# Kernel optimization log

Hardware: AMD Instinct MI355X
Metric: run time of the kernel (lower is better)

The kernel has to match this reference:

```python
import jax, jax.numpy as jnp
import numpy as np

B, T, D, K = 4, 4096, 384, 64

def setup_inputs() -> dict:
    key = jax.random.key(0)
    k1, k2, k3, k4 = jax.random.split(key, 4)
    x = jax.random.normal(k1, (B, T, D), dtype=jnp.float32)
    # nn.Linear weights stored as (out_features, in_features); y = x @ W.T
    Wk = jax.random.normal(k2, (K, D), dtype=jnp.float32) * (1.0 / np.sqrt(D))
    Wq = jax.random.normal(k3, (K, D), dtype=jnp.float32) * (1.0 / np.sqrt(D))
    Wv = jax.random.normal(k4, (D, D), dtype=jnp.float32) * (1.0 / np.sqrt(D))
    return {"x": x, "Wk": Wk, "Wq": Wq, "Wv": Wv}

def reference(x, Wk, Wq, Wv):
    # x: (B,T,D)
    k = jnp.einsum('btd,kd->btk', x, Wk)   # (B,T,K)
    q = jnp.einsum('btd,kd->btk', x, Wq)   # (B,T,K)
    v = jnp.einsum('btd,ed->bte', x, Wv)   # (B,T,D)
    scores = jnp.einsum('btk,bsk->bts', q, k)  # (B,T,T)
    Tq = x.shape[1]
    causal = jnp.tril(jnp.ones((Tq, Tq), dtype=bool))[None, :, :]
    scores = jnp.where(causal, scores, -jnp.inf)
    w = jax.nn.softmax(scores / jnp.sqrt(jnp.asarray(Wk.shape[0], scores.dtype)), axis=-1)
    return jnp.einsum('bts,bsd->btd', w, v)  # (B,T,D)
```

## Files before the change

### kernel.cpp

```cpp
#include <hip/hip_runtime.h>


#define BB 4
#define TT 4096
#define DD 384

#define OWKA 0
#define OWQA 24576
#define OWVB 49152
#define OYK  196608
#define OYQ  1245184
#define OVT  2293760

#define C_EXP 0.18033688011112042f

typedef __bf16 bf16x8 __attribute__((ext_vector_type(8)));
typedef float f32x16 __attribute__((ext_vector_type(16)));
typedef unsigned short u16x4 __attribute__((ext_vector_type(4)));

__device__ __forceinline__ unsigned short f2bf(float f) {
  unsigned int u = __builtin_bit_cast(unsigned int, f);
  u += 0x7FFFu + ((u >> 16) & 1u);
  return (unsigned short)(u >> 16);
}

__device__ __forceinline__ bf16x8 ldb8(const unsigned short* p) {
  return *reinterpret_cast<const bf16x8*>(p);
}

__global__ __launch_bounds__(256) void convert_w(
    const float* __restrict__ Wk, const float* __restrict__ Wq,
    const float* __restrict__ Wv, unsigned short* __restrict__ ws) {
  int g = blockIdx.x * 256 + threadIdx.x;
  int row = g / 96;
  int fin = (g - row * 96) * 4;
  const float* src;
  unsigned short* dstbase;
  int m;
  if (row < 64)       { src = Wk + row * 384;         dstbase = ws + OWKA; m = row; }
  else if (row < 128) { src = Wq + (row - 64) * 384;  dstbase = ws + OWQA; m = row - 64; }
  else                { src = Wv + (row - 128) * 384; dstbase = ws + OWVB; m = row - 128; }
  float4 f = *reinterpret_cast<const float4*>(src + fin);
  u16x4 o;
  o[0] = f2bf(f.x); o[1] = f2bf(f.y); o[2] = f2bf(f.z); o[3] = f2bf(f.w);
  unsigned short* dst = dstbase + (m >> 5) * 12288 + (fin >> 4) * 512
                        + ((((fin >> 3) & 1) << 5) + (m & 31)) * 8 + (fin & 7);
  *reinterpret_cast<u16x4*>(dst) = o;
}

__global__ __launch_bounds__(512) void proj_fused(
    const float* __restrict__ x, const unsigned short* __restrict__ ws_r,
    unsigned short* __restrict__ Yk, unsigned short* __restrict__ Yq,
    unsigned short* __restrict__ Vt) {
  __shared__ __align__(16) unsigned short xlds[12288];
  int tb2 = blockIdx.x;
  int b = tb2 >> 7;
  int tt = tb2 & 127;
  int tid = threadIdx.x;
  {
    const float* xb = x + tb2 * 12288;
#pragma unroll
    for (int j = 0; j < 6; j++) {
      int v = tid + 512 * j;
      int r = v / 96;
      int fin = (v - r * 96) * 4;
      float4 f = *reinterpret_cast<const float4*>(xb + v * 4);
      u16x4 o;
      o[0] = f2bf(f.x); o[1] = f2bf(f.y); o[2] = f2bf(f.z); o[3] = f2bf(f.w);
      unsigned short* dst = xlds + (fin >> 4) * 512
                            + ((((fin >> 3) & 1) << 5) + r) * 8 + (fin & 7);
      *reinterpret_cast<u16x4*>(dst) = o;
    }
  }
  __syncthreads();
  int wid = tid >> 6, lane = tid & 63;
  int l31 = lane & 31, h8 = lane >> 5;
  const f32x16 fz16 = {};
  if (wid < 2) {
    const unsigned short* Wa = ws_r + (wid ? OWQA : OWKA) + lane * 8;
    unsigned short* Ysel = (wid ? Yq : Yk);
    f32x16 acc0 = fz16, acc1 = fz16;
    bf16x8 cw0[8], cw1[8], nw0[8], nw1[8];
#pragma unroll
    for (int i = 0; i < 8; i++) {
      cw0[i] = ldb8(Wa + i * 512);
      cw1[i] = ldb8(Wa + 12288 + i * 512);
    }
    asm volatile("" ::: "memory");
#pragma unroll
    for (int c = 0; c < 3; c++) {
      if (c < 2) {
#pragma unroll
        for (int i = 0; i < 8; i++) {
          nw0[i] = ldb8(Wa + (c + 1) * 4096 + i * 512);
          nw1[i] = ldb8(Wa + 12288 + (c + 1) * 4096 + i * 512);
        }
        asm volatile("" ::: "memory");
      }
#pragma unroll
      for (int i = 0; i < 8; i++) {
        bf16x8 b0 = ldb8(xlds + (c * 8 + i) * 512 + lane * 8);
        acc0 = __builtin_amdgcn_mfma_f32_32x32x16_bf16(cw0[i], b0, acc0, 0, 0, 0);
        acc1 = __builtin_amdgcn_mfma_f32_32x32x16_bf16(cw1[i], b0, acc1, 0, 0, 0);
      }
      if (c < 2) {
#pragma unroll
        for (int i = 0; i < 8; i++) { cw0[i] = nw0[i]; cw1[i] = nw1[i]; }
      }
    }
    int tile = b * 128 + tt;
    f32x16 am[2] = {acc0, acc1};
#pragma unroll
    for (int mt = 0; mt < 2; mt++)
#pragma unroll
      for (int rg = 0; rg < 4; rg++) {
        u16x4 o;
#pragma unroll
        for (int i = 0; i < 4; i++) o[i] = f2bf(am[mt][rg * 4 + i]);
        *reinterpret_cast<u16x4*>(Ysel + tile * 2048 + (mt * 2 + (rg >> 1)) * 512
                                  + (((rg & 1) << 5) + l31) * 8 + 4 * h8) = o;
      }
  } else {
    int vw = wid - 2;
    const unsigned short* Wb = ws_r + OWVB + vw * 2 * 12288 + lane * 8;
    f32x16 acc0 = fz16, acc1 = fz16;
    bf16x8 cw0[8], cw1[8], nw0[8], nw1[8];
#pragma unroll
    for (int i = 0; i < 8; i++) {
      cw0[i] = ldb8(Wb + i * 512);
      cw1[i] = ldb8(Wb + 12288 + i * 512);
    }
    asm volatile("" ::: "memory");
#pragma unroll
    for (int c = 0; c < 3; c++) {
      if (c < 2) {
#pragma unroll
        for (int i = 0; i < 8; i++) {
          nw0[i] = ldb8(Wb + (c + 1) * 4096 + i * 512);
          nw1[i] = ldb8(Wb + 12288 + (c + 1) * 4096 + i * 512);
        }
        asm volatile("" ::: "memory");
      }
#pragma unroll
      for (int i = 0; i < 8; i++) {
        bf16x8 a0 = ldb8(xlds + (c * 8 + i) * 512 + lane * 8);
        acc0 = __builtin_amdgcn_mfma_f32_32x32x16_bf16(a0, cw0[i], acc0, 0, 0, 0);
        acc1 = __builtin_amdgcn_mfma_f32_32x32x16_bf16(a0, cw1[i], acc1, 0, 0, 0);
      }
      if (c < 2) {
#pragma unroll
        for (int i = 0; i < 8; i++) { cw0[i] = nw0[i]; cw1[i] = nw1[i]; }
      }
    }
    int k128 = tt >> 2;
    int ks0 = (tb2 & 3) * 2;
    f32x16 ad[2] = {acc0, acc1};
#pragma unroll
    for (int dt = 0; dt < 2; dt++) {
      int dti = vw * 2 + dt;
      unsigned short* vbase = Vt + ((b * 12 + dti) * 32 + k128) * 4096;
#pragma unroll
      for (int rg = 0; rg < 4; rg++) {
        u16x4 o;
#pragma unroll
        for (int i = 0; i < 4; i++) o[i] = f2bf(ad[dt][rg * 4 + i]);
        int kseg = ks0 + (rg >> 1);
        *reinterpret_cast<u16x4*>(vbase + kseg * 512
                                  + (((rg & 1) << 5) + l31) * 8 + 4 * h8) = o;
      }
    }
  }
}

__global__ __launch_bounds__(256, 2) void flash_attn(
    const unsigned short* __restrict__ Yk, const unsigned short* __restrict__ Yq,
    const unsigned short* __restrict__ Vt, float* __restrict__ out) {
  __shared__ __align__(16) unsigned short pbuf[2][8192];
  __shared__ float lred[4][32];
  int blk = blockIdx.x;
  int xcd = blk & 7;
  int b = xcd >> 1, half = xcd & 1;
  int n = blk >> 3;
  int st = (n < 32) ? (127 - 2 * n - half) : (2 * (n - 32) + half);
  int wid = threadIdx.x >> 6, lane = threadIdx.x & 63;
  int l31 = lane & 31, h8 = lane >> 5;
  const f32x16 fz16 = {};
  const unsigned short* qbase = Yq + (b * 128 + st) * 2048 + lane * 8;
  bf16x8 qf[4];
#pragma unroll
  for (int ks = 0; ks < 4; ks++) qf[ks] = ldb8(qbase + ks * 512);
  f32x16 acc[3];
  acc[0] = fz16; acc[1] = fz16; acc[2] = fz16;
  float psum = 0.f;
  int n128 = (st >> 2) + 1;
  int qrow = st * 32 + l31;
  const unsigned short* kbase = Yk + (b * 128 + wid) * 2048 + lane * 8;
  const unsigned short* vbase = Vt + ((b * 12 + wid * 3) * 32) * 4096 + lane * 8;
#pragma unroll 1
  for (int kb = 0; kb < n128; kb++) {
    const unsigned short* kt = kbase + kb * 8192;
    bf16x8 kf[4];
#pragma unroll
    for (int ks = 0; ks < 4; ks++) kf[ks] = ldb8(kt + ks * 512);
    f32x16 sacc = fz16;
#pragma unroll
    for (int ks = 0; ks < 4; ks++)
      sacc = __builtin_amdgcn_mfma_f32_32x32x16_bf16(kf[ks], qf[ks], sacc, 0, 0, 0);
    int kg0 = kb * 128 + wid * 32 + 4 * h8;
    unsigned short* pw = pbuf[kb & 1];
#pragma unroll
    for (int rg = 0; rg < 4; rg++) {
      u16x4 o;
#pragma unroll
      for (int i = 0; i < 4; i++) {
        int key = kg0 + rg * 8 + i;
        float pv = (key > qrow) ? 0.f : exp2f(sacc[rg * 4 + i] * C_EXP);
        psum += pv;
        o[i] = f2bf(pv);
      }
      int g = wid * 2 + (rg >> 1);
      *reinterpret_cast<u16x4*>(pw + g * 512 + ((rg & 1) * 32 + l31) * 8 + 4 * h8) = o;
    }
    const unsigned short* vt = vbase + kb * 4096;
    bf16x8 vf0[8], vf1[8], vf2[8];
#pragma unroll
    for (int g = 0; g < 8; g++) vf0[g] = ldb8(vt + g * 512);
#pragma unroll
    for (int g = 0; g < 8; g++) vf1[g] = ldb8(vt + 32 * 4096 + g * 512);
#pragma unroll
    for (int g = 0; g < 8; g++) vf2[g] = ldb8(vt + 64 * 4096 + g * 512);
    __syncthreads();
    bf16x8 pf[8];
#pragma unroll
    for (int g = 0; g < 8; g++) pf[g] = ldb8(pw + g * 512 + lane * 8);
#pragma unroll
    for (int g = 0; g < 8; g++) {
      acc[0] = __builtin_amdgcn_mfma_f32_32x32x16_bf16(vf0[g], pf[g], acc[0], 0, 0, 0);
      acc[1] = __builtin_amdgcn_mfma_f32_32x32x16_bf16(vf1[g], pf[g], acc[1], 0, 0, 0);
      acc[2] = __builtin_amdgcn_mfma_f32_32x32x16_bf16(vf2[g], pf[g], acc[2], 0, 0, 0);
    }
  }
  psum += __shfl_xor(psum, 32);
  if (h8 == 0) lred[wid][l31] = psum;
  __syncthreads();
  float lt = lred[0][l31] + lred[1][l31] + lred[2][l31] + lred[3][l31];
  float inv = 1.0f / lt;
  float* ob = out + (b * TT + st * 32 + l31) * DD + wid * 96;
#pragma unroll
  for (int dt = 0; dt < 3; dt++)
#pragma unroll
    for (int rg = 0; rg < 4; rg++) {
      float4 o4;
      o4.x = acc[dt][rg * 4 + 0] * inv; o4.y = acc[dt][rg * 4 + 1] * inv;
      o4.z = acc[dt][rg * 4 + 2] * inv; o4.w = acc[dt][rg * 4 + 3] * inv;
      *reinterpret_cast<float4*>(ob + dt * 32 + rg * 8 + h8 * 4) = o4;
    }
}

extern "C" void kernel_launch(void* const* d_in, const int* in_sizes, int n_in,
                              void* d_out, int out_size, void* d_ws, size_t ws_size,
                              hipStream_t stream) {
  const float* x  = (const float*)d_in[0];
  const float* Wk = (const float*)d_in[1];
  const float* Wq = (const float*)d_in[2];
  const float* Wv = (const float*)d_in[3];
  unsigned short* ws = (unsigned short*)d_ws;
  unsigned short* Yk = ws + OYK;
  unsigned short* Yq = ws + OYQ;
  unsigned short* Vt = ws + OVT;

  convert_w<<<192, 256, 0, stream>>>(Wk, Wq, Wv, ws);
  proj_fused<<<512, 512, 0, stream>>>(x, ws, Yk, Yq, Vt);
  flash_attn<<<512, 256, 0, stream>>>(Yk, Yq, Vt, (float*)d_out);
}
```

Measured before the change: 149.3 us.

## Software-pipeline K and V global loads one key block ahead in attention loop

Loads K and V fragments for the first key block before the loop, then issues the next block's K loads after the score MFMAs and the next block's V loads after the PV MFMAs. This keeps global-memory latency off the critical path of each iteration. It also swaps __syncthreads for an explicit lgkmcnt wait plus s_barrier, so the barrier no longer waits on outstanding global loads. In exchange it keeps many more registers live (double-buffered K and V fragments), which may lower occupancy, and it does one redundant reload on the last iteration.

```diff
diff --git a/kernel.cpp b/kernel.cpp
--- a/kernel.cpp
+++ b/kernel.cpp
@@ -196,16 +196,29 @@
   int qrow = st * 32 + l31;
   const unsigned short* kbase = Yk + (b * 128 + wid) * 2048 + lane * 8;
   const unsigned short* vbase = Vt + ((b * 12 + wid * 3) * 32) * 4096 + lane * 8;
+  bf16x8 kf[4];
+#pragma unroll
+  for (int ks = 0; ks < 4; ks++) kf[ks] = ldb8(kbase + ks * 512);
+  bf16x8 vf0[8], vf1[8], vf2[8];
+#pragma unroll
+  for (int g = 0; g < 8; g++) vf0[g] = ldb8(vbase + g * 512);
+#pragma unroll
+  for (int g = 0; g < 8; g++) vf1[g] = ldb8(vbase + 32 * 4096 + g * 512);
+#pragma unroll
+  for (int g = 0; g < 8; g++) vf2[g] = ldb8(vbase + 64 * 4096 + g * 512);
+  asm volatile("" ::: "memory");
 #pragma unroll 1
   for (int kb = 0; kb < n128; kb++) {
-    const unsigned short* kt = kbase + kb * 8192;
-    bf16x8 kf[4];
-#pragma unroll
-    for (int ks = 0; ks < 4; ks++) kf[ks] = ldb8(kt + ks * 512);
     f32x16 sacc = fz16;
 #pragma unroll
     for (int ks = 0; ks < 4; ks++)
       sacc = __builtin_amdgcn_mfma_f32_32x32x16_bf16(kf[ks], qf[ks], sacc, 0, 0, 0);
+    int kn = (kb + 1 < n128) ? kb + 1 : kb;
+    const unsigned short* ktn = kbase + kn * 8192;
+    bf16x8 kfn[4];
+#pragma unroll
+    for (int ks = 0; ks < 4; ks++) kfn[ks] = ldb8(ktn + ks * 512);
+    asm volatile("" ::: "memory");
     int kg0 = kb * 128 + wid * 32 + 4 * h8;
     unsigned short* pw = pbuf[kb & 1];
 #pragma unroll
@@ -221,15 +234,9 @@
       int g = wid * 2 + (rg >> 1);
       *reinterpret_cast<u16x4*>(pw + g * 512 + ((rg & 1) * 32 + l31) * 8 + 4 * h8) = o;
     }
-    const unsigned short* vt = vbase + kb * 4096;
-    bf16x8 vf0[8], vf1[8], vf2[8];
-#pragma unroll
-    for (int g = 0; g < 8; g++) vf0[g] = ldb8(vt + g * 512);
-#pragma unroll
-    for (int g = 0; g < 8; g++) vf1[g] = ldb8(vt + 32 * 4096 + g * 512);
-#pragma unroll
-    for (int g = 0; g < 8; g++) vf2[g] = ldb8(vt + 64 * 4096 + g * 512);
-    __syncthreads();
+    asm volatile("s_waitcnt lgkmcnt(0)" ::: "memory");
+    __builtin_amdgcn_s_barrier();
+    asm volatile("" ::: "memory");
     bf16x8 pf[8];
 #pragma unroll
     for (int g = 0; g < 8; g++) pf[g] = ldb8(pw + g * 512 + lane * 8);
@@ -239,6 +246,16 @@
       acc[1] = __builtin_amdgcn_mfma_f32_32x32x16_bf16(vf1[g], pf[g], acc[1], 0, 0, 0);
       acc[2] = __builtin_amdgcn_mfma_f32_32x32x16_bf16(vf2[g], pf[g], acc[2], 0, 0, 0);
     }
+    const unsigned short* vtn = vbase + kn * 4096;
+#pragma unroll
+    for (int g = 0; g < 8; g++) vf0[g] = ldb8(vtn + g * 512);
+#pragma unroll
+    for (int g = 0; g < 8; g++) vf1[g] = ldb8(vtn + 32 * 4096 + g * 512);
+#pragma unroll
+    for (int g = 0; g < 8; g++) vf2[g] = ldb8(vtn + 64 * 4096 + g * 512);
+    asm volatile("" ::: "memory");
+#pragma unroll
+    for (int ks = 0; ks < 4; ks++) kf[ks] = kfn[ks];
   }
   psum += __shfl_xor(psum, 32);
   if (h8 == 0) lred[wid][l31] = psum;
```

Measured after the change: 145.5 us. -2.5%, faster.

## Split long causal strips between paired blocks with flag-synchronized partial merge

Applied to the files above, without the earlier changes.

Each long query strip's key-block range is split so the paired short-strip block computes the tail portion after finishing its own strip. The helper writes unnormalized partial outputs and row sums to global memory and sets a flag, and the long-strip block spin-waits on that flag before merging and normalizing. The goal is to balance per-block work across the causal triangle so the longest blocks no longer bound kernel time. The cost is a global spin-wait and extra global round-trips. It also relies on both blocks of a pair being co-resident, otherwise it can deadlock.

```diff
diff --git a/kernel.cpp b/kernel.cpp
--- a/kernel.cpp
+++ b/kernel.cpp
@@ -11,6 +11,7 @@
 #define OYK  196608
 #define OYQ  1245184
 #define OVT  2293760
+#define OSYN 8585216
 
 #define C_EXP 0.18033688011112042f
 
@@ -31,6 +32,10 @@
 __global__ __launch_bounds__(256) void convert_w(
     const float* __restrict__ Wk, const float* __restrict__ Wq,
     const float* __restrict__ Wv, unsigned short* __restrict__ ws) {
+  if (blockIdx.x == 0 && threadIdx.x < 256) {
+    unsigned int* flags = (unsigned int*)((float*)(ws + OSYN) + 8192);
+    flags[threadIdx.x] = 0u;
+  }
   int g = blockIdx.x * 256 + threadIdx.x;
   int row = g / 96;
   int fin = (g - row * 96) * 4;
@@ -172,89 +177,178 @@
   }
 }
 
+__device__ __forceinline__ void strip_visits(
+    const unsigned short* __restrict__ Yk, const unsigned short* __restrict__ Yq,
+    const unsigned short* __restrict__ Vt, int b, int st, int kb0, int kb1,
+    int wid, int lane, unsigned short (*pbuf)[8192], f32x16 acc[3], float& psum) {
+  int l31 = lane & 31, h8 = lane >> 5;
+  const f32x16 fz16 = {};
+  const unsigned short* qbase = Yq + (b * 128 + st) * 2048 + lane * 8;
+  bf16x8 qf[4];
+#pragma unroll
+  for (int ks = 0; ks < 4; ks++) qf[ks] = ldb8(qbase + ks * 512);
+  int qrow = st * 32 + l31;
+  const unsigned short* kbase = Yk + (b * 128 + wid) * 2048 + lane * 8;
+  const unsigned short* vbase = Vt + ((b * 12 + wid * 3) * 32) * 4096 + lane * 8;
+#pragma unroll 1
+  for (int kb = kb0; kb < kb1; kb++) {
+    const unsigned short* kt = kbase + kb * 8192;
+    bf16x8 kf[4];
+#pragma unroll
+    for (int ks = 0; ks < 4; ks++) kf[ks] = ldb8(kt + ks * 512);
+    f32x16 sacc = fz16;
+#pragma unroll
+    for (int ks = 0; ks < 4; ks++)
+      sacc = __builtin_amdgcn_mfma_f32_32x32x16_bf16(kf[ks], qf[ks], sacc, 0, 0, 0);
+    int kg0 = kb * 128 + wid * 32 + 4 * h8;
+    unsigned short* pw = pbuf[kb & 1];
+#pragma unroll
+    for (int rg = 0; rg < 4; rg++) {
+      u16x4 o;
+#pragma unroll
+      for (int i = 0; i < 4; i++) {
+        int key = kg0 + rg * 8 + i;
+        float pv = (key > qrow) ? 0.f : exp2f(sacc[rg * 4 + i] * C_EXP);
+        psum += pv;
+        o[i] = f2bf(pv);
+      }
+      int g = wid * 2 + (rg >> 1);
+      *reinterpret_cast<u16x4*>(pw + g * 512 + ((rg & 1) * 32 + l31) * 8 + 4 * h8) = o;
+    }
+    const unsigned short* vt = vbase + kb * 4096;
+    bf16x8 vf0[8], vf1[8], vf2[8];
+#pragma unroll
+    for (int g = 0; g < 8; g++) vf0[g] = ldb8(vt + g * 512);
+#pragma unroll
+    for (int g = 0; g < 8; g++) vf1[g] = ldb8(vt + 32 * 4096 + g * 512);
+#pragma unroll
+    for (int g = 0; g < 8; g++) vf2[g] = ldb8(vt + 64 * 4096 + g * 512);
+    __syncthreads();
+    bf16x8 pf[8];
+#pragma unroll
+    for (int g = 0; g < 8; g++) pf[g] = ldb8(pw + g * 512 + lane * 8);
+#pragma unroll
+    for (int g = 0; g < 8; g++) {
+      acc[0] = __builtin_amdgcn_mfma_f32_32x32x16_bf16(vf0[g], pf[g], acc[0], 0, 0, 0);
+      acc[1] = __builtin_amdgcn_mfma_f32_32x32x16_bf16(vf1[g], pf[g], acc[1], 0, 0, 0);
+      acc[2] = __builtin_amdgcn_mfma_f32_32x32x16_bf16(vf2[g], pf[g], acc[2], 0, 0, 0);
+    }
+  }
+}
+
 __global__ __launch_bounds__(256, 2) void flash_attn(
     const unsigned short* __restrict__ Yk, const unsigned short* __restrict__ Yq,
-    const unsigned short* __restrict__ Vt, float* __restrict__ out) {
+    const unsigned short* __restrict__ Vt, float* __restrict__ out,
+    unsigned short* __restrict__ ws) {
   __shared__ __align__(16) unsigned short pbuf[2][8192];
   __shared__ float lred[4][32];
   int blk = blockIdx.x;
   int xcd = blk & 7;
   int b = xcd >> 1, half = xcd & 1;
   int n = blk >> 3;
-  int st = (n < 32) ? (127 - 2 * n - half) : (2 * (n - 32) + half);
-  int wid = threadIdx.x >> 6, lane = threadIdx.x & 63;
+  bool isLong = (n < 32);
+  int np = isLong ? n : n - 32;
+  int stL = 127 - 2 * np - half;
+  int stS = 2 * np + half;
+  int nL = (stL >> 2) + 1, nS = (stS >> 2) + 1;
+  int H = (nL + nS + 1) >> 1;
+  if (H > nL) H = nL;
+  int help = nL - H;
+  float* wsf = (float*)(ws + OSYN);
+  unsigned int* flags = (unsigned int*)(wsf + 8192);
+  int pair = xcd * 32 + np;
+  int tid = threadIdx.x;
+  int wid = tid >> 6, lane = tid & 63;
   int l31 = lane & 31, h8 = lane >> 5;
   const f32x16 fz16 = {};
-  const unsigned short* qbase = Yq + (b * 128 + st) * 2048 + lane * 8;
-  bf16x8 qf[4];
-#pragma unroll
-  for (int ks = 0; ks < 4; ks++) qf[ks] = ldb8(qbase + ks * 512);
-  f32x16 acc[3];
-  acc[0] = fz16; acc[1] = fz16; acc[2] = fz16;
-  float psum = 0.f;
-  int n128 = (st >> 2) + 1;
-  int qrow = st * 32 + l31;
-  const unsigned short* kbase = Yk + (b * 128 + wid) * 2048 + lane * 8;
-  const unsigned short* vbase = Vt + ((b * 12 + wid * 3) * 32) * 4096 + lane * 8;
-#pragma unroll 1
-  for (int kb = 0; kb < n128; kb++) {
-    const unsigned short* kt = kbase + kb * 8192;
-    bf16x8 kf[4];
-#pragma unroll
-    for (int ks = 0; ks < 4; ks++) kf[ks] = ldb8(kt + ks * 512);
-    f32x16 sacc = fz16;
-#pragma unroll
-    for (int ks = 0; ks < 4; ks++)
-      sacc = __builtin_amdgcn_mfma_f32_32x32x16_bf16(kf[ks], qf[ks], sacc, 0, 0, 0);
-    int kg0 = kb * 128 + wid * 32 + 4 * h8;
-    unsigned short* pw = pbuf[kb & 1];
-#pragma unroll
-    for (int rg = 0; rg < 4; rg++) {
-      u16x4 o;
-#pragma unroll
-      for (int i = 0; i < 4; i++) {
-        int key = kg0 + rg * 8 + i;
-        float pv = (key > qrow) ? 0.f : exp2f(sacc[rg * 4 + i] * C_EXP);
-        psum += pv;
-        o[i] = f2bf(pv);
-      }
-      int g = wid * 2 + (rg >> 1);
-      *reinterpret_cast<u16x4*>(pw + g * 512 + ((rg & 1) * 32 + l31) * 8 + 4 * h8) = o;
-    }
-    const unsigned short* vt = vbase + kb * 4096;
-    bf16x8 vf0[8], vf1[8], vf2[8];
-#pragma unroll
-    for (int g = 0; g < 8; g++) vf0[g] = ldb8(vt + g * 512);
-#pragma unroll
-    for (int g = 0; g < 8; g++) vf1[g] = ldb8(vt + 32 * 4096 + g * 512);
-#pragma unroll
-    for (int g = 0; g < 8; g++) vf2[g] = ldb8(vt + 64 * 4096 + g * 512);
+
+  if (isLong) {
+    f32x16 acc[3]; acc[0] = fz16; acc[1] = fz16; acc[2] = fz16;
+    float psum = 0.f;
+    strip_visits(Yk, Yq, Vt, b, stL, 0, H, wid, lane, pbuf, acc, psum);
+    psum += __shfl_xor(psum, 32);
+    if (h8 == 0) lred[wid][l31] = psum;
     __syncthreads();
-    bf16x8 pf[8];
-#pragma unroll
-    for (int g = 0; g < 8; g++) pf[g] = ldb8(pw + g * 512 + lane * 8);
-#pragma unroll
-    for (int g = 0; g < 8; g++) {
-      acc[0] = __builtin_amdgcn_mfma_f32_32x32x16_bf16(vf0[g], pf[g], acc[0], 0, 0, 0);
-      acc[1] = __builtin_amdgcn_mfma_f32_32x32x16_bf16(vf1[g], pf[g], acc[1], 0, 0, 0);
-      acc[2] = __builtin_amdgcn_mfma_f32_32x32x16_bf16(vf2[g], pf[g], acc[2], 0, 0, 0);
-    }
-  }
-  psum += __shfl_xor(psum, 32);
-  if (h8 == 0) lred[wid][l31] = psum;
-  __syncthreads();
-  float lt = lred[0][l31] + lred[1][l31] + lred[2][l31] + lred[3][l31];
-  float inv = 1.0f / lt;
-  float* ob = out + (b * TT + st * 32 + l31) * DD + wid * 96;
-#pragma unroll
-  for (int dt = 0; dt < 3; dt++)
-#pragma unroll
-    for (int rg = 0; rg < 4; rg++) {
-      float4 o4;
-      o4.x = acc[dt][rg * 4 + 0] * inv; o4.y = acc[dt][rg * 4 + 1] * inv;
-      o4.z = acc[dt][rg * 4 + 2] * inv; o4.w = acc[dt][rg * 4 + 3] * inv;
-      *reinterpret_cast<float4*>(ob + dt * 32 + rg * 8 + h8 * 4) = o4;
-    }
+    float lt = lred[0][l31] + lred[1][l31] + lred[2][l31] + lred[3][l31];
+    float* ob = out + (b * TT + stL * 32 + l31) * DD + wid * 96;
+    if (help > 0) {
+      if (tid == 0) {
+        while (atomicAdd(&flags[pair], 0u) == 0u) __builtin_amdgcn_s_sleep(32);
+      }
+      __syncthreads();
+      __threadfence();
+      lt += wsf[pair * 32 + l31];
+      float inv = 1.0f / lt;
+#pragma unroll
+      for (int dt = 0; dt < 3; dt++)
+#pragma unroll
+        for (int rg = 0; rg < 4; rg++) {
+          float4 pp = *reinterpret_cast<const float4*>(ob + dt * 32 + rg * 8 + h8 * 4);
+          float4 o4;
+          o4.x = (acc[dt][rg * 4 + 0] + pp.x) * inv;
+          o4.y = (acc[dt][rg * 4 + 1] + pp.y) * inv;
+          o4.z = (acc[dt][rg * 4 + 2] + pp.z) * inv;
+          o4.w = (acc[dt][rg * 4 + 3] + pp.w) * inv;
+          *reinterpret_cast<float4*>(ob + dt * 32 + rg * 8 + h8 * 4) = o4;
+        }
+    } else {
+      float inv = 1.0f / lt;
+#pragma unroll
+      for (int dt = 0; dt < 3; dt++)
+#pragma unroll
+        for (int rg = 0; rg < 4; rg++) {
+          float4 o4;
+          o4.x = acc[dt][rg * 4 + 0] * inv; o4.y = acc[dt][rg * 4 + 1] * inv;
+          o4.z = acc[dt][rg * 4 + 2] * inv; o4.w = acc[dt][rg * 4 + 3] * inv;
+          *reinterpret_cast<float4*>(ob + dt * 32 + rg * 8 + h8 * 4) = o4;
+        }
+    }
+  } else {
+    {
+      f32x16 acc[3]; acc[0] = fz16; acc[1] = fz16; acc[2] = fz16;
+      float psum = 0.f;
+      strip_visits(Yk, Yq, Vt, b, stS, 0, nS, wid, lane, pbuf, acc, psum);
+      psum += __shfl_xor(psum, 32);
+      if (h8 == 0) lred[wid][l31] = psum;
+      __syncthreads();
+      float lt = lred[0][l31] + lred[1][l31] + lred[2][l31] + lred[3][l31];
+      float inv = 1.0f / lt;
+      float* ob = out + (b * TT + stS * 32 + l31) * DD + wid * 96;
+#pragma unroll
+      for (int dt = 0; dt < 3; dt++)
+#pragma unroll
+        for (int rg = 0; rg < 4; rg++) {
+          float4 o4;
+          o4.x = acc[dt][rg * 4 + 0] * inv; o4.y = acc[dt][rg * 4 + 1] * inv;
+          o4.z = acc[dt][rg * 4 + 2] * inv; o4.w = acc[dt][rg * 4 + 3] * inv;
+          *reinterpret_cast<float4*>(ob + dt * 32 + rg * 8 + h8 * 4) = o4;
+        }
+    }
+    if (help > 0) {
+      __syncthreads();
+      f32x16 acc[3]; acc[0] = fz16; acc[1] = fz16; acc[2] = fz16;
+      float psum = 0.f;
+      strip_visits(Yk, Yq, Vt, b, stL, H, nL, wid, lane, pbuf, acc, psum);
+      psum += __shfl_xor(psum, 32);
+      if (h8 == 0) lred[wid][l31] = psum;
+      __syncthreads();
+      float ltb = lred[0][l31] + lred[1][l31] + lred[2][l31] + lred[3][l31];
+      float* ob = out + (b * TT + stL * 32 + l31) * DD + wid * 96;
+#pragma unroll
+      for (int dt = 0; dt < 3; dt++)
+#pragma unroll
+        for (int rg = 0; rg < 4; rg++) {
+          float4 o4;
+          o4.x = acc[dt][rg * 4 + 0]; o4.y = acc[dt][rg * 4 + 1];
+          o4.z = acc[dt][rg * 4 + 2]; o4.w = acc[dt][rg * 4 + 3];
+          *reinterpret_cast<float4*>(ob + dt * 32 + rg * 8 + h8 * 4) = o4;
+        }
+      if (wid == 0 && lane < 32) wsf[pair * 32 + lane] = ltb;
+      __threadfence();
+      __syncthreads();
+      if (tid == 0) atomicExch(&flags[pair], 1u);
+    }
+  }
 }
 
 extern "C" void kernel_launch(void* const* d_in, const int* in_sizes, int n_in,
@@ -271,5 +365,5 @@
 
   convert_w<<<192, 256, 0, stream>>>(Wk, Wq, Wv, ws);
   proj_fused<<<512, 512, 0, stream>>>(x, ws, Yk, Yq, Vt);
-  flash_attn<<<512, 256, 0, stream>>>(Yk, Yq, Vt, (float*)d_out);
-}
+  flash_attn<<<512, 256, 0, stream>>>(Yk, Yq, Vt, (float*)d_out, ws);
+}
```

New measurement: 216.7 us. +45.2%, slower.
